# Performance work log

Hardware: AMD Instinct MI355X
Metric: run time of the kernel (lower is better)

Reference implementation:

```python
import jax, jax.numpy as jnp
import numpy as np

B, W, R, D = 2, 4096, 8, 32


def setup_inputs() -> dict:
    key = jax.random.key(0)
    k1, k2, k3 = jax.random.split(key, 3)
    q_alpha = jax.random.normal(k1, (B, W, R), dtype=jnp.float32)
    k = jax.random.normal(k2, (B, W, R), dtype=jnp.float32)
    h_norm = jax.random.normal(k3, (B, W, D), dtype=jnp.float32)
    # RetNet-style decay rates per rank channel: gamma_i = 1 - 2^{-(6+i)} in (0, 1)
    gamma_vec = 1.0 - jnp.exp2(-(6.0 + jnp.arange(R, dtype=jnp.float32)))
    idx = jnp.arange(W)
    decay_diff = (idx[:, None] - idx[None, :]).astype(jnp.float32)  # [W, W], i - j
    causal_mask = (idx[:, None] >= idx[None, :]).astype(jnp.float32)  # [W, W] lower-tri
    return {
        "q_alpha": q_alpha,
        "k": k,
        "h_norm": h_norm,
        "gamma_vec": gamma_vec,
        "causal_mask": causal_mask,
        "decay_diff": decay_diff,
    }


def reference(q_alpha, k, h_norm, gamma_vec, causal_mask, decay_diff):
    # q_alpha, k: [B, W, R]; h_norm: [B, W, D]; gamma_vec: [R]; masks: [W, W]
    window = h_norm.shape[1]
    kh = k[..., :, None] * h_norm[..., None, :]  # [B, W, R, D]
    dist = decay_diff[:window, :window][..., None]  # [W, W, 1]
    log_gamma = jnp.log(jnp.clip(gamma_vec, 1e-8, None)).reshape(1, 1, -1)  # [1, 1, R]
    causal = causal_mask[:window, :window][..., None]  # [W, W, 1]
    decay_mask = jnp.exp(dist * log_gamma) * causal  # [W, W, R]
    causal_inner = jnp.einsum("ijr,bjrd->bird", decay_mask, kh)  # [B, W, R, D]
    return jnp.einsum("bwr,bwrd->bwd", q_alpha, causal_inner)  # [B, W, D]
```

## Files before the change

kernel.cpp:

```cpp
#include <hip/hip_runtime.h>

#define B 2
#define W 4096
#define R 8
#define D 32
#define L 64
#define C (W / L)

__global__ __launch_bounds__(256) void k_local(const float* __restrict__ kin,
                                               const float* __restrict__ hin,
                                               const float* __restrict__ gamma_vec,
                                               float* __restrict__ ws_state) {
    __shared__ float sk[L][R];
    __shared__ float sh[L][D];
    const int blk = blockIdx.x;
    const int b = blk / C, c = blk % C;
    const int t = threadIdx.x;
    const float* kp = kin + ((size_t)b * W + (size_t)c * L) * R;
    const float* hp = hin + ((size_t)b * W + (size_t)c * L) * D;
    for (int idx = t; idx < L * R; idx += 256) sk[idx / R][idx % R] = kp[idx];
    for (int idx = t; idx < L * D; idx += 256) sh[idx / D][idx % D] = hp[idx];
    __syncthreads();
    const int r = t >> 5;
    const int d = t & 31;
    const float g = gamma_vec[r];
    float S = 0.f;
#pragma unroll
    for (int j = 0; j < L; ++j) {
        S = S * g + sk[j][r] * sh[j][d];
    }
    ws_state[((size_t)(b * C + c) * R + r) * D + d] = S;
}

__global__ __launch_bounds__(256) void k_scan(const float* __restrict__ gamma_vec,
                                              float* __restrict__ ws_state) {
    const int tid = blockIdx.x * 256 + threadIdx.x;
    const int b = tid >> 8;
    const int rd = tid & 255;
    const int r = rd >> 5;
    float gL = gamma_vec[r];
#pragma unroll
    for (int s = 0; s < 6; ++s) gL *= gL;
    float S = 0.f;
    float* base = ws_state + (size_t)b * C * R * D + rd;
    for (int c = 0; c < C; ++c) {
        const float v = base[(size_t)c * R * D];
        base[(size_t)c * R * D] = S;
        S = S * gL + v;
    }
}

__global__ __launch_bounds__(256) void k_out(const float* __restrict__ qin,
                                             const float* __restrict__ kin,
                                             const float* __restrict__ hin,
                                             const float* __restrict__ gamma_vec,
                                             const float* __restrict__ ws_state,
                                             float* __restrict__ out) {
    __shared__ float sq[L][R];
    __shared__ float sk[L][R];
    __shared__ float sh[L][D];
    __shared__ float sA[L][L];
    __shared__ float spow[R][L + 1];
    __shared__ float s0[R][D];
    const int blk = blockIdx.x;
    const int b = blk / C, c = blk % C;
    const int t = threadIdx.x;
    const size_t row0 = (size_t)b * W + (size_t)c * L;
    const float* qp = qin + row0 * R;
    const float* kp = kin + row0 * R;
    const float* hp = hin + row0 * D;
    for (int idx = t; idx < L * R; idx += 256) {
        sq[idx / R][idx % R] = qp[idx];
        sk[idx / R][idx % R] = kp[idx];
    }
    for (int idx = t; idx < L * D; idx += 256) sh[idx / D][idx % D] = hp[idx];
    s0[t >> 5][t & 31] = ws_state[(size_t)(b * C + c) * R * D + t];
    if (t < R) {
        const float g = gamma_vec[t];
        float p = 1.f;
        for (int dl = 0; dl <= L; ++dl) { spow[t][dl] = p; p *= g; }
    }
    __syncthreads();

    for (int e = t; e < L * L; e += 256) {
        const int i = e >> 6, j = e & 63;
        float a = 0.f;
        if (j <= i) {
#pragma unroll
            for (int r = 0; r < R; ++r) a += sq[i][r] * sk[j][r] * spow[r][i - j];
        }
        sA[i][j] = a;
    }
    __syncthreads();

    const int d = t & 31;
    const int ig = t >> 5;
    float acc[8];
#pragma unroll
    for (int s = 0; s < 8; ++s) {
        const int i = ig * 8 + s;
        float a = 0.f;
#pragma unroll
        for (int r = 0; r < R; ++r) a += sq[i][r] * spow[r][i + 1] * s0[r][d];
        acc[s] = a;
    }
    for (int j = 0; j < L; ++j) {
        const float hv = sh[j][d];
#pragma unroll
        for (int s = 0; s < 8; ++s) acc[s] += sA[ig * 8 + s][j] * hv;
    }
#pragma unroll
    for (int s = 0; s < 8; ++s) {
        const int i = ig * 8 + s;
        out[(row0 + (size_t)i) * D + d] = acc[s];
    }
}

extern "C" void kernel_launch(void* const* d_in, const int* in_sizes, int n_in,
                              void* d_out, int out_size, void* d_ws, size_t ws_size,
                              hipStream_t stream) {
    const float* q  = (const float*)d_in[0];
    const float* k  = (const float*)d_in[1];
    const float* h  = (const float*)d_in[2];
    const float* gv = (const float*)d_in[3];
    float* out = (float*)d_out;
    float* ws  = (float*)d_ws;

    k_local<<<B * C, 256, 0, stream>>>(k, h, gv, ws);
    k_scan <<<2,     256, 0, stream>>>(gv, ws);
    k_out  <<<B * C, 256, 0, stream>>>(q, k, h, gv, ws, out);
}
```

Baseline: 142.3 us.

## Drop serial scan kernel, fold prefix into output kernel, double block threads

Removes the separate chunk-state scan kernel. Each output block now recomputes its own incoming state by looping over all earlier chunk states, which costs O(C) redundant reads per block but eliminates a serial 64-step, 2-block launch. Both kernels move to 512 threads: the local-state recurrence is split into even and odd halves with gamma squared, and the output kernel uses a transposed, padded A matrix read as float4, skipping the causally zero upper columns. Vectorised float4 loads replace the strided staging loops.

```diff
diff --git a/kernel.cpp b/kernel.cpp
--- a/kernel.cpp
+++ b/kernel.cpp
@@ -7,59 +7,49 @@
 #define L 64
 #define C (W / L)
 
-__global__ __launch_bounds__(256) void k_local(const float* __restrict__ kin,
+__global__ __launch_bounds__(512) void k_local(const float* __restrict__ kin,
                                                const float* __restrict__ hin,
                                                const float* __restrict__ gamma_vec,
                                                float* __restrict__ ws_state) {
     __shared__ float sk[L][R];
     __shared__ float sh[L][D];
+    __shared__ float part[2][R][D];
     const int blk = blockIdx.x;
     const int b = blk / C, c = blk % C;
     const int t = threadIdx.x;
     const float* kp = kin + ((size_t)b * W + (size_t)c * L) * R;
     const float* hp = hin + ((size_t)b * W + (size_t)c * L) * D;
-    for (int idx = t; idx < L * R; idx += 256) sk[idx / R][idx % R] = kp[idx];
-    for (int idx = t; idx < L * D; idx += 256) sh[idx / D][idx % D] = hp[idx];
+    ((float*)sk)[t] = kp[t];
+    ((float4*)sh)[t] = ((const float4*)hp)[t];
     __syncthreads();
-    const int r = t >> 5;
-    const int d = t & 31;
+    const int half = t >> 8;
+    const int rd = t & 255;
+    const int r = rd >> 5, d = rd & 31;
     const float g = gamma_vec[r];
+    const float g2 = g * g;
     float S = 0.f;
 #pragma unroll
-    for (int j = 0; j < L; ++j) {
-        S = S * g + sk[j][r] * sh[j][d];
+    for (int m = 0; m < 32; ++m) {
+        const int j = 2 * m + half;
+        S = S * g2 + sk[j][r] * sh[j][d];
     }
-    ws_state[((size_t)(b * C + c) * R + r) * D + d] = S;
-}
-
-__global__ __launch_bounds__(256) void k_scan(const float* __restrict__ gamma_vec,
-                                              float* __restrict__ ws_state) {
-    const int tid = blockIdx.x * 256 + threadIdx.x;
-    const int b = tid >> 8;
-    const int rd = tid & 255;
-    const int r = rd >> 5;
-    float gL = gamma_vec[r];
-#pragma unroll
-    for (int s = 0; s < 6; ++s) gL *= gL;
-    float S = 0.f;
-    float* base = ws_state + (size_t)b * C * R * D + rd;
-    for (int c = 0; c < C; ++c) {
-        const float v = base[(size_t)c * R * D];
-        base[(size_t)c * R * D] = S;
-        S = S * gL + v;
+    part[half][r][d] = S;
+    __syncthreads();
+    if (t < 256) {
+        ws_state[(size_t)(b * C + c) * R * D + rd] = part[1][r][d] + g * part[0][r][d];
     }
 }
 
-__global__ __launch_bounds__(256) void k_out(const float* __restrict__ qin,
+__global__ __launch_bounds__(512) void k_out(const float* __restrict__ qin,
                                              const float* __restrict__ kin,
                                              const float* __restrict__ hin,
                                              const float* __restrict__ gamma_vec,
                                              const float* __restrict__ ws_state,
                                              float* __restrict__ out) {
-    __shared__ float sq[L][R];
+    __shared__ float sq[L][R + 1];
     __shared__ float sk[L][R];
     __shared__ float sh[L][D];
-    __shared__ float sA[L][L];
+    __shared__ __align__(16) float sAT[L][L + 4];
     __shared__ float spow[R][L + 1];
     __shared__ float s0[R][D];
     const int blk = blockIdx.x;
@@ -69,12 +59,9 @@
     const float* qp = qin + row0 * R;
     const float* kp = kin + row0 * R;
     const float* hp = hin + row0 * D;
-    for (int idx = t; idx < L * R; idx += 256) {
-        sq[idx / R][idx % R] = qp[idx];
-        sk[idx / R][idx % R] = kp[idx];
-    }
-    for (int idx = t; idx < L * D; idx += 256) sh[idx / D][idx % D] = hp[idx];
-    s0[t >> 5][t & 31] = ws_state[(size_t)(b * C + c) * R * D + t];
+    sq[t >> 3][t & 7] = qp[t];
+    sk[t >> 3][t & 7] = kp[t];
+    ((float4*)sh)[t] = ((const float4*)hp)[t];
     if (t < R) {
         const float g = gamma_vec[t];
         float p = 1.f;
@@ -82,38 +69,53 @@
     }
     __syncthreads();
 
-    for (int e = t; e < L * L; e += 256) {
-        const int i = e >> 6, j = e & 63;
+    if (t < 256) {
+        const int r = t >> 5;
+        float gL = gamma_vec[r];
+#pragma unroll
+        for (int s = 0; s < 6; ++s) gL *= gL;
+        float P = 0.f;
+        const float* wsp = ws_state + (size_t)b * C * R * D + t;
+        for (int cc = 0; cc < c; ++cc)
+            P = P * gL + wsp[(size_t)cc * R * D];
+        s0[r][t & 31] = P;
+    }
+
+    for (int e = t; e < L * L; e += 512) {
+        const int j = e >> 6, i = e & 63;
         float a = 0.f;
         if (j <= i) {
 #pragma unroll
             for (int r = 0; r < R; ++r) a += sq[i][r] * sk[j][r] * spow[r][i - j];
         }
-        sA[i][j] = a;
+        sAT[j][i] = a;
     }
     __syncthreads();
 
     const int d = t & 31;
     const int ig = t >> 5;
-    float acc[8];
+    float pr[R];
 #pragma unroll
-    for (int s = 0; s < 8; ++s) {
-        const int i = ig * 8 + s;
+    for (int r = 0; r < R; ++r) pr[r] = s0[r][d];
+    float acc[4];
+#pragma unroll
+    for (int s = 0; s < 4; ++s) {
+        const int i = ig * 4 + s;
         float a = 0.f;
 #pragma unroll
-        for (int r = 0; r < R; ++r) a += sq[i][r] * spow[r][i + 1] * s0[r][d];
+        for (int r = 0; r < R; ++r) a += sq[i][r] * spow[r][i + 1] * pr[r];
         acc[s] = a;
     }
-    for (int j = 0; j < L; ++j) {
+    const int jmax = ig * 4 + 3;
+    for (int j = 0; j <= jmax; ++j) {
         const float hv = sh[j][d];
-#pragma unroll
-        for (int s = 0; s < 8; ++s) acc[s] += sA[ig * 8 + s][j] * hv;
+        const float4 av = *(const float4*)&sAT[j][ig * 4];
+        acc[0] += av.x * hv; acc[1] += av.y * hv;
+        acc[2] += av.z * hv; acc[3] += av.w * hv;
     }
 #pragma unroll
-    for (int s = 0; s < 8; ++s) {
-        const int i = ig * 8 + s;
-        out[(row0 + (size_t)i) * D + d] = acc[s];
-    }
+    for (int s = 0; s < 4; ++s)
+        out[(row0 + (size_t)(ig * 4 + s)) * D + d] = acc[s];
 }
 
 extern "C" void kernel_launch(void* const* d_in, const int* in_sizes, int n_in,
@@ -126,7 +128,6 @@
     float* out = (float*)d_out;
     float* ws  = (float*)d_ws;
 
-    k_local<<<B * C, 256, 0, stream>>>(k, h, gv, ws);
-    k_scan <<<2,     256, 0, stream>>>(gv, ws);
-    k_out  <<<B * C, 256, 0, stream>>>(q, k, h, gv, ws, out);
+    k_local<<<B * C, 512, 0, stream>>>(k, h, gv, ws);
+    k_out  <<<B * C, 512, 0, stream>>>(q, k, h, gv, ws, out);
 }
```

Result: slower. 148.0 us (+4.1%).
